# Performance work log

Measured on AMD Instinct MI355X. Metric: run time of the kernel, lower is better.

## Reference

```python
import jax, jax.numpy as jnp
import numpy as np

N_NODES = 100000
N_EDGES = 1600000
IN_DIM, HID, OUT = 128, 64, 32


def setup_inputs() -> dict:
    key = jax.random.key(0)
    ks = jax.random.split(key, 8)
    x = jax.random.normal(ks[0], (N_NODES, IN_DIM), dtype=jnp.float32)
    edge_index = jax.random.randint(ks[1], (2, N_EDGES), 0, N_NODES, dtype=jnp.int64)
    # Glorot-ish init for weights, zeros for biases (PyG GCNConv convention)
    def glorot(k, fan_in, fan_out):
        s = jnp.sqrt(6.0 / (fan_in + fan_out)).astype(jnp.float32)
        return jax.random.uniform(k, (fan_in, fan_out), jnp.float32, -s, s)
    return {
        "x": x,
        "edge_index": edge_index,
        "W1": glorot(ks[2], IN_DIM, HID), "b1": jnp.zeros((HID,), jnp.float32),
        "W2": glorot(ks[3], HID, HID),    "b2": jnp.zeros((HID,), jnp.float32),
        "W3": glorot(ks[4], HID, OUT),    "b3": jnp.zeros((OUT,), jnp.float32),
    }


def _gcn_layer(x, W, b, src, dst, dinv, n_nodes):
    # GCNConv with add_self_loops=True, symmetric normalization.
    h = x @ W                                   # [N, F_out]
    norm = dinv[src] * dinv[dst]                # [E]
    msg = h[src] * norm[:, None]                # gather + scale, [E, F_out]
    agg = jax.ops.segment_sum(msg, dst, num_segments=n_nodes)
    agg = agg + (dinv * dinv)[:, None] * h      # self-loop term, norm = dinv_i^2
    return agg + b


def reference(x, edge_index, W1, b1, W2, b2, W3, b3):
    n = x.shape[0]
    src, dst = edge_index[0], edge_index[1]
    # degree over targets, including the self loop (+1)
    deg = jax.ops.segment_sum(jnp.ones_like(dst, dtype=x.dtype), dst, num_segments=n) + 1.0
    dinv = deg ** -0.5
    h = jax.nn.relu(_gcn_layer(x, W1, b1, src, dst, dinv, n))
    # dropout is identity in eval mode
    h = jax.nn.relu(_gcn_layer(h, W2, b2, src, dst, dinv, n))
    return _gcn_layer(h, W3, b3, src, dst, dinv, n)
```

## Files before the change

### kernel.cpp

```cpp
#include <hip/hip_runtime.h>


#define BLK 256
#define SCAN_CHUNK 1024
#define BSHIFT 8
#define BMASK 255
#define BCAP 6144
#define BCH 4096

__device__ __forceinline__ float bf2f(unsigned short u) {
    return __uint_as_float(((unsigned int)u) << 16);
}
__device__ __forceinline__ unsigned short f2bf(float f) {
    unsigned int x = __float_as_uint(f);
    unsigned int r = (x + 0x7FFFu + ((x >> 16) & 1u)) >> 16;
    return (unsigned short)r;
}

__global__ __launch_bounds__(256) void bucket_kernel(const int* __restrict__ src,
                                                     const int* __restrict__ dst,
                                                     int* __restrict__ bcur,
                                                     unsigned int* __restrict__ bbuf,
                                                     int E, int NB) {
    __shared__ int hist[512];
    __shared__ int base_[512];
    const int tid = threadIdx.x;
    const int e0 = blockIdx.x * BCH;
    const int e1 = min(e0 + BCH, E);
    for (int i = tid; i < NB; i += 256) hist[i] = 0;
    __syncthreads();
    for (int e = e0 + tid; e < e1; e += 256)
        atomicAdd(&hist[dst[e] >> BSHIFT], 1);
    __syncthreads();
    for (int i = tid; i < NB; i += 256) {
        int c = hist[i];
        base_[i] = c ? atomicAdd(&bcur[i], c) : 0;
        hist[i] = 0;
    }
    __syncthreads();
    for (int e = e0 + tid; e < e1; e += 256) {
        int d = dst[e];
        int b = d >> BSHIFT;
        int idx = base_[b] + atomicAdd(&hist[b], 1);
        if (idx < BCAP)
            bbuf[(size_t)b * BCAP + idx] =
                ((unsigned int)src[e] << BSHIFT) | (unsigned int)(d & BMASK);
    }
}

__global__ __launch_bounds__(256) void bdeg_kernel(const int* __restrict__ bcur,
                                                   const unsigned int* __restrict__ bbuf,
                                                   int* __restrict__ degi, int N) {
    __shared__ int hist[256];
    const int b = blockIdx.x;
    const int tid = threadIdx.x;
    hist[tid] = 0;
    __syncthreads();
    const int cnt = min(bcur[b], BCAP);
    const unsigned int* p = bbuf + (size_t)b * BCAP;
    for (int i = tid; i < cnt; i += 256)
        atomicAdd(&hist[p[i] & BMASK], 1);
    __syncthreads();
    const int node = (b << BSHIFT) + tid;
    if (node < N) degi[node] = hist[tid];
}

__global__ void dinv_kernel(const int* __restrict__ degi, float* __restrict__ dinv, int N) {
    int i = blockIdx.x * blockDim.x + threadIdx.x;
    if (i < N) dinv[i] = rsqrtf((float)degi[i] + 1.0f);
}

__global__ __launch_bounds__(256) void scanA_kernel(const int* __restrict__ degi,
                                                    int* __restrict__ bsum, int N) {
    const int t = threadIdx.x;
    const int base = blockIdx.x * SCAN_CHUNK + t * 4;
    int s = 0;
#pragma unroll
    for (int j = 0; j < 4; ++j) { int i = base + j; if (i < N) s += degi[i]; }
    __shared__ int red[256];
    red[t] = s;
    __syncthreads();
    for (int off = 128; off > 0; off >>= 1) {
        if (t < off) red[t] += red[t + off];
        __syncthreads();
    }
    if (t == 0) bsum[blockIdx.x] = red[0];
}

__global__ __launch_bounds__(256) void scanB_kernel(const int* __restrict__ bsum,
                                                    int* __restrict__ boff,
                                                    int* __restrict__ rowptr_last, int NBLK) {
    __shared__ int sh[256];
    const int t = threadIdx.x;
    sh[t] = (t < NBLK) ? bsum[t] : 0;
    __syncthreads();
    for (int off = 1; off < 256; off <<= 1) {
        int u = (t >= off) ? sh[t - off] : 0;
        __syncthreads();
        sh[t] += u;
        __syncthreads();
    }
    if (t < NBLK) boff[t] = (t == 0) ? 0 : sh[t - 1];
    if (t == 0) *rowptr_last = sh[255];
}

__global__ __launch_bounds__(256) void scanC_kernel(const int* __restrict__ degi,
                                                    const int* __restrict__ boff,
                                                    int* __restrict__ rowptr, int N) {
    const int t = threadIdx.x;
    const int base = blockIdx.x * SCAN_CHUNK + t * 4;
    int loc[4];
    int s = 0;
#pragma unroll
    for (int j = 0; j < 4; ++j) {
        int i = base + j;
        loc[j] = (i < N) ? degi[i] : 0;
        s += loc[j];
    }
    __shared__ int sh[256];
    sh[t] = s;
    __syncthreads();
    for (int off = 1; off < 256; off <<= 1) {
        int u = (t >= off) ? sh[t - off] : 0;
        __syncthreads();
        sh[t] += u;
        __syncthreads();
    }
    int ex = ((t == 0) ? 0 : sh[t - 1]) + boff[blockIdx.x];
#pragma unroll
    for (int j = 0; j < 4; ++j) {
        int i = base + j;
        if (i < N) { rowptr[i] = ex; ex += loc[j]; }
    }
}

__global__ __launch_bounds__(256) void bfill_kernel(const int* __restrict__ bcur,
                                                    const unsigned int* __restrict__ bbuf,
                                                    const int* __restrict__ rowptr,
                                                    const float* __restrict__ dinv,
                                                    int2* __restrict__ epack, int N) {
    __shared__ int cur[256];
    __shared__ float sdinv[256];
    const int b = blockIdx.x;
    const int tid = threadIdx.x;
    const int node = (b << BSHIFT) + tid;
    cur[tid] = (node < N) ? rowptr[node] : 0;
    sdinv[tid] = (node < N) ? dinv[node] : 0.f;
    __syncthreads();
    const int cnt = min(bcur[b], BCAP);
    const unsigned int* p = bbuf + (size_t)b * BCAP;
    for (int i = tid; i < cnt; i += 256) {
        unsigned int v = p[i];
        int s = (int)(v >> BSHIFT);
        int dl = (int)(v & BMASK);
        int slot = atomicAdd(&cur[dl], 1);
        epack[slot] = make_int2(s << 7, __float_as_int(dinv[s] * sdinv[dl]));
    }
}

template<int K, int C, int RT>
__global__ __launch_bounds__(256) void gemm_kernel(const float* __restrict__ X,
                                                   const float* __restrict__ W,
                                                   unsigned short* __restrict__ Y, int N) {
    constexpr int CG = C / 4;
    constexpr int RG = 256 / CG;
    constexpr int ROWS = RG * RT;
    __shared__ float Wl[K * C];
    __shared__ float Xl[ROWS * (K + 1)];
    const int tid = threadIdx.x;

    for (int i = tid; i < K * C / 4; i += 256)
        ((float4*)Wl)[i] = ((const float4*)W)[i];

    const int row0 = blockIdx.x * ROWS;
    for (int idx = tid; idx < ROWS * (K / 4); idx += 256) {
        int r = idx / (K / 4), kc = idx % (K / 4);
        float4 v = make_float4(0.f, 0.f, 0.f, 0.f);
        int gr = row0 + r;
        if (gr < N) v = ((const float4*)X)[(size_t)gr * (K / 4) + kc];
        float* p = &Xl[r * (K + 1) + kc * 4];
        p[0] = v.x; p[1] = v.y; p[2] = v.z; p[3] = v.w;
    }
    __syncthreads();

    const int cg = tid % CG, rg = tid / CG;
    float acc[RT][4];
#pragma unroll
    for (int j = 0; j < RT; ++j)
#pragma unroll
        for (int c = 0; c < 4; ++c) acc[j][c] = 0.f;

#pragma unroll 4
    for (int k = 0; k < K; ++k) {
        float4 w = *(const float4*)&Wl[k * C + cg * 4];
#pragma unroll
        for (int j = 0; j < RT; ++j) {
            float xv = Xl[(rg * RT + j) * (K + 1) + k];
            acc[j][0] += xv * w.x;
            acc[j][1] += xv * w.y;
            acc[j][2] += xv * w.z;
            acc[j][3] += xv * w.w;
        }
    }

#pragma unroll
    for (int j = 0; j < RT; ++j) {
        int gr = row0 + rg * RT + j;
        if (gr < N) {
            ushort4 o;
            o.x = f2bf(acc[j][0]); o.y = f2bf(acc[j][1]);
            o.z = f2bf(acc[j][2]); o.w = f2bf(acc[j][3]);
            *(ushort4*)&Y[(size_t)gr * C + cg * 4] = o;
        }
    }
}

template<int C>
__device__ __forceinline__ float gath(const char* __restrict__ Hb, int ex, int foff) {
    unsigned o = (C == 64) ? (unsigned)ex : ((unsigned)ex >> 1);
    return bf2f(*(const unsigned short*)(Hb + o + foff));
}

template<int C, bool RELU>
__global__ __launch_bounds__(256) void agg_kernel(const unsigned short* __restrict__ H,
                                                  const int* __restrict__ rowptr,
                                                  const int2* __restrict__ epack,
                                                  const float* __restrict__ dinv,
                                                  const float* __restrict__ bias,
                                                  float* __restrict__ OUT, int N) {
    constexpr int NPB = 256 / C;
    const int f = threadIdx.x % C;
    const int node = blockIdx.x * NPB + threadIdx.x / C;
    if (node >= N) return;
    const int lo = rowptr[node], hi = rowptr[node + 1];
    const float di = dinv[node];
    const char* Hb = (const char*)H;
    const int foff = f * 2;

    float a0 = 0.f, a1 = 0.f, a2 = 0.f, a3 = 0.f;
    int i = lo;
    if (i + 8 <= hi) {
        int2 e0 = epack[i + 0], e1 = epack[i + 1], e2 = epack[i + 2], e3 = epack[i + 3];
        int2 e4 = epack[i + 4], e5 = epack[i + 5], e6 = epack[i + 6], e7 = epack[i + 7];
        for (;;) {
            const int inext = i + 8;
            const bool more = (inext + 8 <= hi);
            int2 n0, n1, n2, n3, n4, n5, n6, n7;
            if (more) {
                n0 = epack[inext + 0]; n1 = epack[inext + 1];
                n2 = epack[inext + 2]; n3 = epack[inext + 3];
                n4 = epack[inext + 4]; n5 = epack[inext + 5];
                n6 = epack[inext + 6]; n7 = epack[inext + 7];
            }
            float h0 = gath<C>(Hb, e0.x, foff);
            float h1 = gath<C>(Hb, e1.x, foff);
            float h2 = gath<C>(Hb, e2.x, foff);
            float h3 = gath<C>(Hb, e3.x, foff);
            float h4 = gath<C>(Hb, e4.x, foff);
            float h5 = gath<C>(Hb, e5.x, foff);
            float h6 = gath<C>(Hb, e6.x, foff);
            float h7 = gath<C>(Hb, e7.x, foff);
            a0 = fmaf(h0, __int_as_float(e0.y), a0);
            a1 = fmaf(h1, __int_as_float(e1.y), a1);
            a2 = fmaf(h2, __int_as_float(e2.y), a2);
            a3 = fmaf(h3, __int_as_float(e3.y), a3);
            a0 = fmaf(h4, __int_as_float(e4.y), a0);
            a1 = fmaf(h5, __int_as_float(e5.y), a1);
            a2 = fmaf(h6, __int_as_float(e6.y), a2);
            a3 = fmaf(h7, __int_as_float(e7.y), a3);
            i = inext;
            if (!more) break;
            e0 = n0; e1 = n1; e2 = n2; e3 = n3;
            e4 = n4; e5 = n5; e6 = n6; e7 = n7;
        }
    }
    for (; i + 4 <= hi; i += 4) {
        int2 e0 = epack[i + 0], e1 = epack[i + 1], e2 = epack[i + 2], e3 = epack[i + 3];
        float h0 = gath<C>(Hb, e0.x, foff);
        float h1 = gath<C>(Hb, e1.x, foff);
        float h2 = gath<C>(Hb, e2.x, foff);
        float h3 = gath<C>(Hb, e3.x, foff);
        a0 = fmaf(h0, __int_as_float(e0.y), a0);
        a1 = fmaf(h1, __int_as_float(e1.y), a1);
        a2 = fmaf(h2, __int_as_float(e2.y), a2);
        a3 = fmaf(h3, __int_as_float(e3.y), a3);
    }
    for (; i < hi; ++i) {
        int2 e0 = epack[i];
        a0 = fmaf(gath<C>(Hb, e0.x, foff), __int_as_float(e0.y), a0);
    }

    float r = (a0 + a1) + (a2 + a3)
            + di * di * bf2f(H[(size_t)node * C + f])
            + bias[f];
    if (RELU) r = fmaxf(r, 0.f);
    OUT[(size_t)node * C + f] = r;
}

extern "C" void kernel_launch(void* const* d_in, const int* in_sizes, int n_in,
                              void* d_out, int out_size, void* d_ws, size_t ws_size,
                              hipStream_t stream) {
    const float* x  = (const float*)d_in[0];
    const int*   ei = (const int*)d_in[1];
    const float* W1 = (const float*)d_in[2];
    const float* b1 = (const float*)d_in[3];
    const float* W2 = (const float*)d_in[4];
    const float* b2 = (const float*)d_in[5];
    const float* W3 = (const float*)d_in[6];
    const float* b3 = (const float*)d_in[7];
    float* out = (float*)d_out;

    const int N = in_sizes[0] / 128;
    const int E = in_sizes[1] / 2;
    const int* src = ei;
    const int* dst = ei + E;
    const int NSCAN = (N + SCAN_CHUNK - 1) / SCAN_CHUNK;
    const int NB = (N + BMASK) >> BSHIFT;
    const int NBB = (E + BCH - 1) / BCH;

    auto align = [](size_t v) { return (v + 255) & ~(size_t)255; };
    char* wsb = (char*)d_ws;
    size_t off = 0;
    float* dinv   = (float*)(wsb + off); off += align((size_t)N * 4);
    int*   rowptr = (int*)  (wsb + off); off += align((size_t)(N + 1) * 4);
    int*   degi   = (int*)  (wsb + off); off += align((size_t)N * 4);
    int*   bcur   = (int*)  (wsb + off); off += align((size_t)NB * 4);
    int*   bsum   = (int*)  (wsb + off); off += align((size_t)NSCAN * 4);
    int*   boff   = (int*)  (wsb + off); off += align((size_t)NSCAN * 4);
    unsigned int* bbuf = (unsigned int*)(wsb + off); off += align((size_t)NB * BCAP * 4);
    int2*  epack  = (int2*) (wsb + off); off += align((size_t)E * 8);
    unsigned short* P = (unsigned short*)(wsb + off); off += align((size_t)N * 64 * 2);
    float* Q      = (float*)(wsb + off);

    hipMemsetAsync(bcur, 0, (size_t)NB * 4, stream);
    bucket_kernel<<<NBB, 256, 0, stream>>>(src, dst, bcur, bbuf, E, NB);
    bdeg_kernel<<<NB, 256, 0, stream>>>(bcur, bbuf, degi, N);
    dinv_kernel<<<(N + BLK - 1) / BLK, BLK, 0, stream>>>(degi, dinv, N);
    scanA_kernel<<<NSCAN, 256, 0, stream>>>(degi, bsum, N);
    scanB_kernel<<<1, 256, 0, stream>>>(bsum, boff, rowptr + N, NSCAN);
    scanC_kernel<<<NSCAN, 256, 0, stream>>>(degi, boff, rowptr, N);
    bfill_kernel<<<NB, 256, 0, stream>>>(bcur, bbuf, rowptr, dinv, epack, N);

    gemm_kernel<128, 64, 2><<<(N + 31) / 32, BLK, 0, stream>>>(x, W1, P, N);
    agg_kernel<64, true><<<(N * 64 + BLK - 1) / BLK, BLK, 0, stream>>>(P, rowptr, epack,
                                                                       dinv, b1, Q, N);

    gemm_kernel<64, 64, 4><<<(N + 63) / 64, BLK, 0, stream>>>(Q, W2, P, N);
    agg_kernel<64, true><<<(N * 64 + BLK - 1) / BLK, BLK, 0, stream>>>(P, rowptr, epack,
                                                                       dinv, b2, Q, N);

    gemm_kernel<64, 32, 4><<<(N + 127) / 128, BLK, 0, stream>>>(Q, W3, P, N);
    agg_kernel<32, false><<<(N * 32 + BLK - 1) / BLK, BLK, 0, stream>>>(P, rowptr, epack,
                                                                        dinv, b3, out, N);
}
```

Baseline: 408.7 us.

## Use bf16 MFMA GEMMs, bf16 intermediate activations, fuse dinv into degree kernel

```diff
diff --git a/kernel.cpp b/kernel.cpp
--- a/kernel.cpp
+++ b/kernel.cpp
@@ -7,6 +7,9 @@
 #define BMASK 255
 #define BCAP 6144
 #define BCH 4096
+
+typedef __attribute__((ext_vector_type(8))) short short8v;
+typedef __attribute__((ext_vector_type(4))) float f32x4;
 
 __device__ __forceinline__ float bf2f(unsigned short u) {
     return __uint_as_float(((unsigned int)u) << 16);
@@ -50,7 +53,8 @@
 
 __global__ __launch_bounds__(256) void bdeg_kernel(const int* __restrict__ bcur,
                                                    const unsigned int* __restrict__ bbuf,
-                                                   int* __restrict__ degi, int N) {
+                                                   int* __restrict__ degi,
+                                                   float* __restrict__ dinv, int N) {
     __shared__ int hist[256];
     const int b = blockIdx.x;
     const int tid = threadIdx.x;
@@ -62,12 +66,11 @@
         atomicAdd(&hist[p[i] & BMASK], 1);
     __syncthreads();
     const int node = (b << BSHIFT) + tid;
-    if (node < N) degi[node] = hist[tid];
-}
-
-__global__ void dinv_kernel(const int* __restrict__ degi, float* __restrict__ dinv, int N) {
-    int i = blockIdx.x * blockDim.x + threadIdx.x;
-    if (i < N) dinv[i] = rsqrtf((float)degi[i] + 1.0f);
+    if (node < N) {
+        int dg = hist[tid];
+        degi[node] = dg;
+        dinv[node] = rsqrtf((float)dg + 1.0f);
+    }
 }
 
 __global__ __launch_bounds__(256) void scanA_kernel(const int* __restrict__ degi,
@@ -158,59 +161,73 @@
     }
 }
 
-template<int K, int C, int RT>
-__global__ __launch_bounds__(256) void gemm_kernel(const float* __restrict__ X,
-                                                   const float* __restrict__ W,
-                                                   unsigned short* __restrict__ Y, int N) {
-    constexpr int CG = C / 4;
-    constexpr int RG = 256 / CG;
-    constexpr int ROWS = RG * RT;
-    __shared__ float Wl[K * C];
-    __shared__ float Xl[ROWS * (K + 1)];
-    const int tid = threadIdx.x;
-
-    for (int i = tid; i < K * C / 4; i += 256)
-        ((float4*)Wl)[i] = ((const float4*)W)[i];
-
-    const int row0 = blockIdx.x * ROWS;
-    for (int idx = tid; idx < ROWS * (K / 4); idx += 256) {
-        int r = idx / (K / 4), kc = idx % (K / 4);
-        float4 v = make_float4(0.f, 0.f, 0.f, 0.f);
-        int gr = row0 + r;
-        if (gr < N) v = ((const float4*)X)[(size_t)gr * (K / 4) + kc];
-        float* p = &Xl[r * (K + 1) + kc * 4];
-        p[0] = v.x; p[1] = v.y; p[2] = v.z; p[3] = v.w;
-    }
-    __syncthreads();
-
-    const int cg = tid % CG, rg = tid / CG;
-    float acc[RT][4];
-#pragma unroll
-    for (int j = 0; j < RT; ++j)
-#pragma unroll
-        for (int c = 0; c < 4; ++c) acc[j][c] = 0.f;
-
-#pragma unroll 4
-    for (int k = 0; k < K; ++k) {
-        float4 w = *(const float4*)&Wl[k * C + cg * 4];
-#pragma unroll
-        for (int j = 0; j < RT; ++j) {
-            float xv = Xl[(rg * RT + j) * (K + 1) + k];
-            acc[j][0] += xv * w.x;
-            acc[j][1] += xv * w.y;
-            acc[j][2] += xv * w.z;
-            acc[j][3] += xv * w.w;
+__global__ __launch_bounds__(256) void wcvt_kernel(const float* __restrict__ W1,
+                                                   const float* __restrict__ W2,
+                                                   const float* __restrict__ W3,
+                                                   unsigned short* __restrict__ Wt1,
+                                                   unsigned short* __restrict__ Wt2,
+                                                   unsigned short* __restrict__ Wt3) {
+    int i = blockIdx.x * 256 + threadIdx.x;
+    if (i < 8192) {
+        int k = i >> 6, c = i & 63;
+        Wt1[c * 128 + k] = f2bf(W1[i]);
+    } else if (i < 12288) {
+        int j = i - 8192;
+        int k = j >> 6, c = j & 63;
+        Wt2[c * 64 + k] = f2bf(W2[j]);
+    } else if (i < 14336) {
+        int j = i - 12288;
+        int k = j >> 5, c = j & 31;
+        Wt3[c * 64 + k] = f2bf(W3[j]);
+    }
+}
+
+template<int K, int C, bool AF32>
+__global__ __launch_bounds__(256) void gemm_mfma(const void* __restrict__ Xv,
+                                                 const unsigned short* __restrict__ Wt,
+                                                 unsigned short* __restrict__ Y, int N) {
+    constexpr int NS = K / 32;
+    constexpr int NT = C / 16;
+    const int lane = threadIdx.x & 63;
+    const int wave = threadIdx.x >> 6;
+    const int r0 = blockIdx.x * 64 + wave * 16;
+    const int lc = lane & 15;
+    const int kg = (lane >> 4) * 8;
+    const int arow = r0 + lc;
+
+    short8v a[NS];
+#pragma unroll
+    for (int s = 0; s < NS; ++s) {
+        if (arow < N) {
+            if (AF32) {
+                const float* xp = (const float*)Xv + (size_t)arow * K + s * 32 + kg;
+                float4 u = *(const float4*)xp;
+                float4 v = *(const float4*)(xp + 4);
+                unsigned short e[8] = { f2bf(u.x), f2bf(u.y), f2bf(u.z), f2bf(u.w),
+                                        f2bf(v.x), f2bf(v.y), f2bf(v.z), f2bf(v.w) };
+                a[s] = *(const short8v*)e;
+            } else {
+                a[s] = *(const short8v*)((const unsigned short*)Xv
+                                         + (size_t)arow * K + s * 32 + kg);
+            }
+        } else {
+            short8v z = { 0, 0, 0, 0, 0, 0, 0, 0 };
+            a[s] = z;
         }
     }
 
 #pragma unroll
-    for (int j = 0; j < RT; ++j) {
-        int gr = row0 + rg * RT + j;
-        if (gr < N) {
-            ushort4 o;
-            o.x = f2bf(acc[j][0]); o.y = f2bf(acc[j][1]);
-            o.z = f2bf(acc[j][2]); o.w = f2bf(acc[j][3]);
-            *(ushort4*)&Y[(size_t)gr * C + cg * 4] = o;
+    for (int ct = 0; ct < NT; ++ct) {
+        f32x4 acc = { 0.f, 0.f, 0.f, 0.f };
+#pragma unroll
+        for (int s = 0; s < NS; ++s) {
+            short8v b = *(const short8v*)&Wt[(size_t)(ct * 16 + lc) * K + s * 32 + kg];
+            acc = __builtin_amdgcn_mfma_f32_16x16x32_bf16(a[s], b, acc, 0, 0, 0);
+        }
+#pragma unroll
+        for (int i = 0; i < 4; ++i) {
+            int gr = r0 + (lane >> 4) * 4 + i;
+            if (gr < N) Y[(size_t)gr * C + ct * 16 + lc] = f2bf(acc[i]);
         }
     }
 }
@@ -221,13 +238,13 @@
     return bf2f(*(const unsigned short*)(Hb + o + foff));
 }
 
-template<int C, bool RELU>
+template<int C, bool RELU, bool OBF16>
 __global__ __launch_bounds__(256) void agg_kernel(const unsigned short* __restrict__ H,
                                                   const int* __restrict__ rowptr,
                                                   const int2* __restrict__ epack,
                                                   const float* __restrict__ dinv,
                                                   const float* __restrict__ bias,
-                                                  float* __restrict__ OUT, int N) {
+                                                  void* __restrict__ OUT, int N) {
     constexpr int NPB = 256 / C;
     const int f = threadIdx.x % C;
     const int node = blockIdx.x * NPB + threadIdx.x / C;
@@ -239,40 +256,25 @@
 
     float a0 = 0.f, a1 = 0.f, a2 = 0.f, a3 = 0.f;
     int i = lo;
-    if (i + 8 <= hi) {
+    for (; i + 8 <= hi; i += 8) {
         int2 e0 = epack[i + 0], e1 = epack[i + 1], e2 = epack[i + 2], e3 = epack[i + 3];
         int2 e4 = epack[i + 4], e5 = epack[i + 5], e6 = epack[i + 6], e7 = epack[i + 7];
-        for (;;) {
-            const int inext = i + 8;
-            const bool more = (inext + 8 <= hi);
-            int2 n0, n1, n2, n3, n4, n5, n6, n7;
-            if (more) {
-                n0 = epack[inext + 0]; n1 = epack[inext + 1];
-                n2 = epack[inext + 2]; n3 = epack[inext + 3];
-                n4 = epack[inext + 4]; n5 = epack[inext + 5];
-                n6 = epack[inext + 6]; n7 = epack[inext + 7];
-            }
-            float h0 = gath<C>(Hb, e0.x, foff);
-            float h1 = gath<C>(Hb, e1.x, foff);
-            float h2 = gath<C>(Hb, e2.x, foff);
-            float h3 = gath<C>(Hb, e3.x, foff);
-            float h4 = gath<C>(Hb, e4.x, foff);
-            float h5 = gath<C>(Hb, e5.x, foff);
-            float h6 = gath<C>(Hb, e6.x, foff);
-            float h7 = gath<C>(Hb, e7.x, foff);
-            a0 = fmaf(h0, __int_as_float(e0.y), a0);
-            a1 = fmaf(h1, __int_as_float(e1.y), a1);
-            a2 = fmaf(h2, __int_as_float(e2.y), a2);
-            a3 = fmaf(h3, __int_as_float(e3.y), a3);
-            a0 = fmaf(h4, __int_as_float(e4.y), a0);
-            a1 = fmaf(h5, __int_as_float(e5.y), a1);
-            a2 = fmaf(h6, __int_as_float(e6.y), a2);
-            a3 = fmaf(h7, __int_as_float(e7.y), a3);
-            i = inext;
-            if (!more) break;
-            e0 = n0; e1 = n1; e2 = n2; e3 = n3;
-            e4 = n4; e5 = n5; e6 = n6; e7 = n7;
-        }
+        float h0 = gath<C>(Hb, e0.x, foff);
+        float h1 = gath<C>(Hb, e1.x, foff);
+        float h2 = gath<C>(Hb, e2.x, foff);
+        float h3 = gath<C>(Hb, e3.x, foff);
+        float h4 = gath<C>(Hb, e4.x, foff);
+        float h5 = gath<C>(Hb, e5.x, foff);
+        float h6 = gath<C>(Hb, e6.x, foff);
+        float h7 = gath<C>(Hb, e7.x, foff);
+        a0 = fmaf(h0, __int_as_float(e0.y), a0);
+        a1 = fmaf(h1, __int_as_float(e1.y), a1);
+        a2 = fmaf(h2, __int_as_float(e2.y), a2);
+        a3 = fmaf(h3, __int_as_float(e3.y), a3);
+        a0 = fmaf(h4, __int_as_float(e4.y), a0);
+        a1 = fmaf(h5, __int_as_float(e5.y), a1);
+        a2 = fmaf(h6, __int_as_float(e6.y), a2);
+        a3 = fmaf(h7, __int_as_float(e7.y), a3);
     }
     for (; i + 4 <= hi; i += 4) {
         int2 e0 = epack[i + 0], e1 = epack[i + 1], e2 = epack[i + 2], e3 = epack[i + 3];
@@ -294,7 +296,8 @@
             + di * di * bf2f(H[(size_t)node * C + f])
             + bias[f];
     if (RELU) r = fmaxf(r, 0.f);
-    OUT[(size_t)node * C + f] = r;
+    if (OBF16) ((unsigned short*)OUT)[(size_t)node * C + f] = f2bf(r);
+    else       ((float*)OUT)[(size_t)node * C + f] = r;
 }
 
 extern "C" void kernel_launch(void* const* d_in, const int* in_sizes, int n_in,
@@ -329,27 +332,32 @@
     int*   boff   = (int*)  (wsb + off); off += align((size_t)NSCAN * 4);
     unsigned int* bbuf = (unsigned int*)(wsb + off); off += align((size_t)NB * BCAP * 4);
     int2*  epack  = (int2*) (wsb + off); off += align((size_t)E * 8);
-    unsigned short* P = (unsigned short*)(wsb + off); off += align((size_t)N * 64 * 2);
-    float* Q      = (float*)(wsb + off);
-
+    unsigned short* P  = (unsigned short*)(wsb + off); off += align((size_t)N * 64 * 2);
+    unsigned short* Q  = (unsigned short*)(wsb + off); off += align((size_t)N * 64 * 2);
+    unsigned short* Wt1 = (unsigned short*)(wsb + off); off += align((size_t)8192 * 2);
+    unsigned short* Wt2 = (unsigned short*)(wsb + off); off += align((size_t)4096 * 2);
+    unsigned short* Wt3 = (unsigned short*)(wsb + off); off += align((size_t)2048 * 2);
+
+    wcvt_kernel<<<56, 256, 0, stream>>>(W1, W2, W3, Wt1, Wt2, Wt3);
     hipMemsetAsync(bcur, 0, (size_t)NB * 4, stream);
     bucket_kernel<<<NBB, 256, 0, stream>>>(src, dst, bcur, bbuf, E, NB);
-    bdeg_kernel<<<NB, 256, 0, stream>>>(bcur, bbuf, degi, N);
-    dinv_kernel<<<(N + BLK - 1) / BLK, BLK, 0, stream>>>(degi, dinv, N);
+    bdeg_kernel<<<NB, 256, 0, stream>>>(bcur, bbuf, degi, dinv, N);
     scanA_kernel<<<NSCAN, 256, 0, stream>>>(degi, bsum, N);
     scanB_kernel<<<1, 256, 0, stream>>>(bsum, boff, rowptr + N, NSCAN);
     scanC_kernel<<<NSCAN, 256, 0, stream>>>(degi, boff, rowptr, N);
     bfill_kernel<<<NB, 256, 0, stream>>>(bcur, bbuf, rowptr, dinv, epack, N);
 
-    gemm_kernel<128, 64, 2><<<(N + 31) / 32, BLK, 0, stream>>>(x, W1, P, N);
-    agg_kernel<64, true><<<(N * 64 + BLK - 1) / BLK, BLK, 0, stream>>>(P, rowptr, epack,
-                                                                       dinv, b1, Q, N);
-
-    gemm_kernel<64, 64, 4><<<(N + 63) / 64, BLK, 0, stream>>>(Q, W2, P, N);
-    agg_kernel<64, true><<<(N * 64 + BLK - 1) / BLK, BLK, 0, stream>>>(P, rowptr, epack,
-                                                                       dinv, b2, Q, N);
-
-    gemm_kernel<64, 32, 4><<<(N + 127) / 128, BLK, 0, stream>>>(Q, W3, P, N);
-    agg_kernel<32, false><<<(N * 32 + BLK - 1) / BLK, BLK, 0, stream>>>(P, rowptr, epack,
-                                                                        dinv, b3, out, N);
-}
+    const int GB = (N + 63) / 64;
+
+    gemm_mfma<128, 64, true><<<GB, 256, 0, stream>>>(x, Wt1, P, N);
+    agg_kernel<64, true, true><<<(N * 64 + BLK - 1) / BLK, BLK, 0, stream>>>(
+        P, rowptr, epack, dinv, b1, Q, N);
+
+    gemm_mfma<64, 64, false><<<GB, 256, 0, stream>>>(Q, Wt2, P, N);
+    agg_kernel<64, true, true><<<(N * 64 + BLK - 1) / BLK, BLK, 0, stream>>>(
+        P, rowptr, epack, dinv, b2, Q, N);
+
+    gemm_mfma<64, 32, false><<<GB, 256, 0, stream>>>(Q, Wt3, P, N);
+    agg_kernel<32, false, false><<<(N * 32 + BLK - 1) / BLK, BLK, 0, stream>>>(
+        P, rowptr, epack, dinv, b3, out, N);
+}
```

New measurement: 355.6 us. 13.0% less time.
